# Kernel optimization log

Hardware: AMD Instinct MI355X
Metric: run time of the kernel (lower is better)

Reference implementation:

```python
import jax, jax.numpy as jnp
import numpy as np

RES = 64      # resolution (D=H=W)
WIDTH = 32    # FNO channel width
MODES = 8     # retained Fourier modes per dim
NL = 4        # FNO layers
NU = 0.000185 # viscosity
FCH = 128     # projection hidden width
B = 4


def setup_inputs() -> dict:
    key = jax.random.key(0)
    ks = jax.random.split(key, 8)
    u = jax.random.normal(ks[0], (B, 3, RES, RES, RES), jnp.float32)
    s = 1.0 / (WIDTH * WIDTH)
    fc0_w = jax.random.normal(ks[1], (3, WIDTH), jnp.float32) * (1.0 / 3.0) ** 0.5
    fc0_b = jnp.zeros((WIDTH,), jnp.float32)
    # (layer, corner, in, out, m1, m2, m3, re/im)
    spec_w = jax.random.normal(ks[2], (NL, 4, WIDTH, WIDTH, MODES, MODES, MODES, 2), jnp.float32) * s
    w_pw = jax.random.normal(ks[3], (NL, WIDTH, WIDTH), jnp.float32) * (1.0 / WIDTH) ** 0.5
    b_pw = jnp.zeros((NL, WIDTH), jnp.float32)
    fc1_w = jax.random.normal(ks[4], (WIDTH, FCH), jnp.float32) * (1.0 / WIDTH) ** 0.5
    fc1_b = jnp.zeros((FCH,), jnp.float32)
    fc2_w = jax.random.normal(ks[5], (FCH, 6), jnp.float32) * (1.0 / FCH) ** 0.5
    fc2_b = jnp.zeros((6,), jnp.float32)
    return dict(u=u, fc0_w=fc0_w, fc0_b=fc0_b, spec_w=spec_w, w_pw=w_pw,
                b_pw=b_pw, fc1_w=fc1_w, fc1_b=fc1_b, fc2_w=fc2_w, fc2_b=fc2_b)


def _pointwise(x, w, b):
    # 1x1x1 conv: (B,C,D,H,W) x (C,O) -> (B,O,D,H,W)
    return jnp.einsum('bcdhw,co->bodhw', x, w) + b[None, :, None, None, None]


def _spectral_conv(x, wf):
    m = MODES
    Bn, C, D, H, W = x.shape
    ft = jnp.fft.rfftn(x, axes=(-3, -2, -1))           # (B,C,D,H,W//2+1) complex64
    w = wf[..., 0] + 1j * wf[..., 1]                   # (4,C,O,m,m,m)
    mul = lambda blk, ww: jnp.einsum('bixyz,ioxyz->boxyz', blk, ww)
    out = jnp.zeros((Bn, w.shape[2], D, H, W // 2 + 1), jnp.complex64)
    out = out.at[:, :, :m, :m, :m].set(mul(ft[:, :, :m, :m, :m], w[0]))
    out = out.at[:, :, -m:, :m, :m].set(mul(ft[:, :, -m:, :m, :m], w[1]))
    out = out.at[:, :, :m, -m:, :m].set(mul(ft[:, :, :m, -m:, :m], w[2]))
    out = out.at[:, :, -m:, -m:, :m].set(mul(ft[:, :, -m:, -m:, :m], w[3]))
    return jnp.fft.irfftn(out, s=(D, H, W), axes=(-3, -2, -1))


def _fno(u, fc0_w, fc0_b, spec_w, w_pw, b_pw, fc1_w, fc1_b, fc2_w, fc2_b):
    x = _pointwise(u, fc0_w, fc0_b)
    for l in range(NL):
        x1 = _spectral_conv(x, spec_w[l])
        x2 = _pointwise(x, w_pw[l], b_pw[l])
        x = x1 + x2
        if l < NL - 1:
            x = jax.nn.gelu(x)
    x = jax.nn.gelu(_pointwise(x, fc1_w, fc1_b))
    return _pointwise(x, fc2_w, fc2_b)


def _ns_hard_core(u):
    # du/dt = -(u.grad)u + nu * lap(u), periodic central differences
    dx = 2.0 * np.pi / RES
    conv = jnp.zeros_like(u)
    diff = jnp.zeros_like(u)
    for j in range(3):
        ax = 2 + j
        up = jnp.roll(u, -1, axis=ax)
        um = jnp.roll(u, 1, axis=ax)
        du = (up - um) / (2.0 * dx)          # d u_i / d x_j for all i
        conv = conv - u[:, j:j + 1] * du
        diff = diff + (up - 2.0 * u + um) / (dx * dx)
    return conv + NU * diff


def reference(u, fc0_w, fc0_b, spec_w, w_pw, b_pw, fc1_w, fc1_b, fc2_w, fc2_b):
    du_hard = _ns_hard_core(u)
    tau = _fno(u, fc0_w, fc0_b, spec_w, w_pw, b_pw, fc1_w, fc1_b, fc2_w, fc2_b)
    du_dt = du_hard + tau[:, :3] * 0.001
    return du_dt, tau
```

## Files before the change

kernel.cpp:

```cpp
#include <hip/hip_runtime.h>
#include <hip/hip_bf16.h>

#define RES 64
#define WIDTH 32
#define MODES 8
#define R3 262144
#define TWO_PI_OVER_64 0.09817477042468103f

__device__ __forceinline__ float geluf(float x) {
    float g = 1.5957691216057308f * (x + 0.044715f * x * x * x);
    return x * __builtin_amdgcn_rcpf(1.0f + __expf(-g));
}

constexpr double tcos_(double x) {
    double r = 1.0, term = 1.0;
    for (int i = 1; i <= 12; i++) { term *= -x * x / ((2.0 * i - 1.0) * (2.0 * i)); r += term; }
    return r;
}
constexpr double tsin_(double x) {
    double r = x, term = x;
    for (int i = 1; i <= 12; i++) { term *= -x * x / ((2.0 * i) * (2.0 * i + 1.0)); r += term; }
    return r;
}
struct Tw64 { float c[64]; float s[64]; };
constexpr Tw64 mkTw() {
    Tw64 t{};
    const double th = 6.283185307179586476925286766559 / 64.0;
    for (int i = 0; i < 64; i++) {
        double a = th * (i <= 32 ? i : i - 64);
        t.c[i] = (float)tcos_(a);
        t.s[i] = (float)tsin_(a);
    }
    return t;
}
constexpr Tw64 TWT = mkTw();

__global__ void k_fc0(const float* __restrict__ u, const float* __restrict__ w,
                      const float* __restrict__ bias, float* __restrict__ X) {
    __shared__ float ws[96];
    __shared__ float bs[32];
    int t = threadIdx.x;
    if (t < 96) ws[t] = w[t];
    if (t < 32) bs[t] = bias[t];
    __syncthreads();
    size_t s = (size_t)blockIdx.x * 256 + t;
    int b = (int)(s >> 18);
    size_t p = s & (R3 - 1);
    const float* ub = u + (size_t)b * 3 * R3;
    float u0 = ub[p], u1 = ub[R3 + p], u2 = ub[2 * R3 + p];
    float* xb = X + (size_t)b * 32 * R3;
    #pragma unroll
    for (int o = 0; o < 32; o++) {
        xb[(size_t)o * R3 + p] = bs[o] + u0 * ws[o] + u1 * ws[32 + o] + u2 * ws[64 + o];
    }
}

__global__ void __launch_bounds__(256, 6)
k_fwd_zy(const float* __restrict__ X, float2* __restrict__ S2) {
    int t = threadIdx.x;
    int q = t >> 6, y = t & 63;
    int bcx0 = blockIdx.x * 4;
    __shared__ float2 zt[4][8][66];
    __shared__ float2 tw[64];
    if (t < 64) { float s, c; __sincosf(TWO_PI_OVER_64 * t, &s, &c); tw[t] = make_float2(c, s); }

    const float* row = X + (size_t)(bcx0 + q) * 4096 + (size_t)y * 64;
    float re[8], im[8];
    #pragma unroll
    for (int k = 0; k < 8; k++) { re[k] = 0.f; im[k] = 0.f; }
    #pragma unroll
    for (int zb = 0; zb < 8; zb++) {
        float xa[4], xb4[4];
        *(float4*)xa  = *(const float4*)(row + zb * 4);
        *(float4*)xb4 = *(const float4*)(row + zb * 4 + 32);
        #pragma unroll
        for (int j = 0; j < 4; j++) {
            int z = zb * 4 + j;
            float sv = xa[j] + xb4[j];
            float dv = xa[j] - xb4[j];
            #pragma unroll
            for (int k = 0; k < 8; k++) {
                float v = (k & 1) ? dv : sv;
                re[k] += v * TWT.c[(k * z) & 63];
                im[k] -= v * TWT.s[(k * z) & 63];
            }
        }
    }
    #pragma unroll
    for (int k = 0; k < 8; k++) zt[q][k][y] = make_float2(re[k], im[k]);
    __syncthreads();

    int l = t & 63;
    int jy = l >> 2, kp = l & 3;
    int f = jy < 8 ? jy : 48 + jy;
    int k0 = kp * 2;
    float re0 = 0.f, im0 = 0.f, re1 = 0.f, im1 = 0.f;
    #pragma unroll 8
    for (int yy = 0; yy < 64; yy++) {
        float2 w = tw[(f * yy) & 63];
        float2 v0 = zt[q][k0][yy];
        float2 v1 = zt[q][k0 + 1][yy];
        re0 += v0.x * w.x + v0.y * w.y;
        im0 += v0.y * w.x - v0.x * w.y;
        re1 += v1.x * w.x + v1.y * w.y;
        im1 += v1.y * w.x - v1.x * w.y;
    }
    float2* dst = S2 + (size_t)(bcx0 + q) * 128 + jy * 8 + k0;
    dst[0] = make_float2(re0, im0);
    dst[1] = make_float2(re1, im1);
}

__global__ void k_fwd_x(const float2* __restrict__ S2, float2* __restrict__ S3) {
    int bc = blockIdx.x >> 3, kz = blockIdx.x & 7;
    int t = threadIdx.x;
    __shared__ float2 in[64 * 16];
    __shared__ float2 tw[64];
    if (t < 64) { float s, c; __sincosf(TWO_PI_OVER_64 * t, &s, &c); tw[t] = make_float2(c, s); }
    #pragma unroll
    for (int i = 0; i < 4; i++) {
        int e = t + 256 * i;
        in[e] = S2[((size_t)bc * 1024 + e) * 8 + kz];
    }
    __syncthreads();
    int jx = t >> 4, jy = t & 15;
    int f = jx < 8 ? jx : 48 + jx;
    float re = 0.f, im = 0.f;
    for (int x = 0; x < 64; x++) {
        float2 v = in[x * 16 + jy];
        float2 w = tw[(f * x) & 63];
        re += v.x * w.x + v.y * w.y;
        im += v.y * w.x - v.x * w.y;
    }
    S3[(size_t)bc * 2048 + (size_t)t * 8 + kz] = make_float2(re, im);
}

__global__ void k_specmul(const float2* __restrict__ S3, const float* __restrict__ spec_w,
                          float2* __restrict__ S4, int layer) {
    int mp = blockIdx.x;
    int t = threadIdx.x;
    int jxy = mp >> 2;
    int kz0 = (mp & 3) * 2;
    int jy = jxy & 15, jx = jxy >> 4;
    int corner = (jx >= 8 ? 1 : 0) + (jy >= 8 ? 2 : 0);
    int m1 = jx & 7, m2 = jy & 7;
    int mode0 = jxy * 8 + kz0;
    __shared__ float4 W4[1024];
    __shared__ float2 inb[2][128];
    const float* wbase = spec_w + (size_t)layer * 4194304 + (size_t)corner * 1048576
                       + m1 * 128 + m2 * 16 + kz0 * 2;
    #pragma unroll
    for (int j = 0; j < 8; j++) {
        int e = t + 128 * j;
        int i = e >> 5, o = e & 31;
        W4[e] = *(const float4*)(wbase + (size_t)i * 32768 + (size_t)o * 1024);
    }
    inb[0][t] = S3[(size_t)t * 2048 + mode0];
    inb[1][t] = S3[(size_t)t * 2048 + mode0 + 1];
    __syncthreads();
    int b = t >> 5, o = t & 31;
    float re0 = 0.f, im0 = 0.f, re1 = 0.f, im1 = 0.f;
    #pragma unroll 8
    for (int i = 0; i < 32; i++) {
        float2 a0 = inb[0][b * 32 + i];
        float2 a1 = inb[1][b * 32 + i];
        float4 w = W4[i * 32 + o];
        re0 += a0.x * w.x - a0.y * w.y;
        im0 += a0.x * w.y + a0.y * w.x;
        re1 += a1.x * w.z - a1.y * w.w;
        im1 += a1.x * w.w + a1.y * w.z;
    }
    S4[(size_t)(b * 32 + o) * 2048 + mode0]     = make_float2(re0, im0);
    S4[(size_t)(b * 32 + o) * 2048 + mode0 + 1] = make_float2(re1, im1);
}

__global__ void k_inv_x(const float2* __restrict__ S4, float2* __restrict__ S5) {
    int bo = blockIdx.x >> 3, kz = blockIdx.x & 7;
    int t = threadIdx.x;
    __shared__ float2 in[256];
    __shared__ float2 tw[64];
    if (t < 64) { float s, c; __sincosf(TWO_PI_OVER_64 * t, &s, &c); tw[t] = make_float2(c, s); }
    in[t] = S4[(size_t)bo * 2048 + (size_t)t * 8 + kz];
    __syncthreads();
    int x = t & 63, g = t >> 6;
    #pragma unroll
    for (int m = 0; m < 4; m++) {
        int jy = g + 4 * m;
        float re = 0.f, im = 0.f;
        #pragma unroll
        for (int jx = 0; jx < 16; jx++) {
            int f = jx < 8 ? jx : 48 + jx;
            float2 v = in[jx * 16 + jy];
            float2 w = tw[(f * x) & 63];
            re += v.x * w.x - v.y * w.y;
            im += v.x * w.y + v.y * w.x;
        }
        S5[((size_t)bo * 64 + x) * 128 + jy * 8 + kz] = make_float2(re, im);
    }
}

__global__ void __launch_bounds__(256, 3)
k_inv_yz_pw(const float2* __restrict__ S5, const float* __restrict__ w_pw,
            const float* __restrict__ b_pw, float* __restrict__ X,
            int layer, int do_gelu) {
    int blk = blockIdx.x;
    int yg = blk & 3, x = (blk >> 2) & 63, b = blk >> 8;
    int t = threadIdx.x;
    __shared__ float2 s5s[32 * 132];
    __shared__ float2 st[256];
    __shared__ float xt[2048];
    __shared__ float2 tw[64];
    if (t < 64) { float s, c; __sincosf(TWO_PI_OVER_64 * t, &s, &c); tw[t] = make_float2(c, s); }
    #pragma unroll
    for (int i = 0; i < 8; i++) {
        int f4 = t + 256 * i;
        int o = f4 >> 6, j4 = f4 & 63;
        float4 v = ((const float4*)(S5 + ((size_t)(b * 32 + o) * 64 + x) * 128))[j4];
        *(float4*)(&s5s[o * 132 + j4 * 2]) = v;
    }
    __syncthreads();
    int z = t & 63, og = t >> 6;
    int og8 = og * 8;
    int og8u = __builtin_amdgcn_readfirstlane(og8);
    const float* wl = w_pw + layer * 1024 + og8u;
    const float* bl = b_pw + layer * 32 + og8u;
    float bt0 = bl[0], bt1 = bl[1], bt2 = bl[2], bt3 = bl[3];
    float bt4 = bl[4], bt5 = bl[5], bt6 = bl[6], bt7 = bl[7];
    float2 tz1 = tw[z];
    float2 tz2 = tw[(2 * z) & 63];
    float2 tz3 = tw[(3 * z) & 63];
    float2 tz4 = tw[(4 * z) & 63];
    float2 tz5 = tw[(5 * z) & 63];
    float2 tz6 = tw[(6 * z) & 63];
    float2 tz7 = tw[(7 * z) & 63];
    const float inv_n = 1.0f / 262144.0f;
    for (int yi = 0; yi < 16; yi++) {
        int y = yg * 16 + yi;
        {
            int o = t >> 3, k = t & 7;
            float re = 0.f, im = 0.f;
            #pragma unroll
            for (int jy = 0; jy < 16; jy++) {
                int f = jy < 8 ? jy : 48 + jy;
                float2 v = s5s[o * 132 + jy * 8 + k];
                float2 w = tw[(f * y) & 63];
                re += v.x * w.x - v.y * w.y;
                im += v.x * w.y + v.y * w.x;
            }
            st[t] = make_float2(re, im);
        }
        size_t base = (size_t)b * 8388608 + (size_t)(x * 64 + y) * 64;
        #pragma unroll
        for (int i = 0; i < 8; i++) {
            int e = t + 256 * i;
            int c = e >> 6, zz = e & 63;
            xt[e] = X[base + (size_t)c * R3 + zz];
        }
        __syncthreads();
#define INVZ_S(o) (st[(o) * 8 + 0].x \
        + 2.f * (st[(o) * 8 + 1].x * tz1.x - st[(o) * 8 + 1].y * tz1.y) \
        + 2.f * (st[(o) * 8 + 2].x * tz2.x - st[(o) * 8 + 2].y * tz2.y) \
        + 2.f * (st[(o) * 8 + 3].x * tz3.x - st[(o) * 8 + 3].y * tz3.y) \
        + 2.f * (st[(o) * 8 + 4].x * tz4.x - st[(o) * 8 + 4].y * tz4.y) \
        + 2.f * (st[(o) * 8 + 5].x * tz5.x - st[(o) * 8 + 5].y * tz5.y) \
        + 2.f * (st[(o) * 8 + 6].x * tz6.x - st[(o) * 8 + 6].y * tz6.y) \
        + 2.f * (st[(o) * 8 + 7].x * tz7.x - st[(o) * 8 + 7].y * tz7.y))
        float acc0 = bt0 + INVZ_S(og8 + 0) * inv_n;
        float acc1 = bt1 + INVZ_S(og8 + 1) * inv_n;
        float acc2 = bt2 + INVZ_S(og8 + 2) * inv_n;
        float acc3 = bt3 + INVZ_S(og8 + 3) * inv_n;
        float acc4 = bt4 + INVZ_S(og8 + 4) * inv_n;
        float acc5 = bt5 + INVZ_S(og8 + 5) * inv_n;
        float acc6 = bt6 + INVZ_S(og8 + 6) * inv_n;
        float acc7 = bt7 + INVZ_S(og8 + 7) * inv_n;
#undef INVZ_S
        #pragma unroll 4
        for (int c = 0; c < 32; c++) {
            float xc = xt[c * 64 + z];
            const float* wr = wl + c * 32;
            float w0 = wr[0], w1 = wr[1], w2 = wr[2], w3 = wr[3];
            float w4 = wr[4], w5 = wr[5], w6 = wr[6], w7 = wr[7];
            acc0 += xc * w0; acc1 += xc * w1; acc2 += xc * w2; acc3 += xc * w3;
            acc4 += xc * w4; acc5 += xc * w5; acc6 += xc * w6; acc7 += xc * w7;
        }
        __syncthreads();
        float r;
        r = do_gelu ? geluf(acc0) : acc0; X[base + (size_t)(og8 + 0) * R3 + z] = r;
        r = do_gelu ? geluf(acc1) : acc1; X[base + (size_t)(og8 + 1) * R3 + z] = r;
        r = do_gelu ? geluf(acc2) : acc2; X[base + (size_t)(og8 + 2) * R3 + z] = r;
        r = do_gelu ? geluf(acc3) : acc3; X[base + (size_t)(og8 + 3) * R3 + z] = r;
        r = do_gelu ? geluf(acc4) : acc4; X[base + (size_t)(og8 + 4) * R3 + z] = r;
        r = do_gelu ? geluf(acc5) : acc5; X[base + (size_t)(og8 + 5) * R3 + z] = r;
        r = do_gelu ? geluf(acc6) : acc6; X[base + (size_t)(og8 + 6) * R3 + z] = r;
        r = do_gelu ? geluf(acc7) : acc7; X[base + (size_t)(og8 + 7) * R3 + z] = r;
    }
}

#define X32(M) M(0) M(1) M(2) M(3) M(4) M(5) M(6) M(7) M(8) M(9) M(10) M(11) M(12) M(13) \
               M(14) M(15) M(16) M(17) M(18) M(19) M(20) M(21) M(22) M(23) M(24) M(25) \
               M(26) M(27) M(28) M(29) M(30) M(31)
__global__ void __launch_bounds__(256, 2)
k_head(const float* __restrict__ X, const float* __restrict__ w1,
       const float* __restrict__ b1, const float* __restrict__ w2,
       const float* __restrict__ b2, float* __restrict__ tau_out) {
    int t = threadIdx.x;
    size_t s0 = ((size_t)blockIdx.x * 256 + t) * 2;
    int b = (int)(s0 >> 18);
    size_t p = s0 & (R3 - 1);
    const float* xb = X + (size_t)b * 8388608 + p;
#define LOADX(c) float2 v##c = *(const float2*)(xb + (size_t)(c) * R3);
    X32(LOADX)
#undef LOADX
    float acc00 = b2[0], acc01 = b2[1], acc02 = b2[2], acc03 = b2[3], acc04 = b2[4], acc05 = b2[5];
    float acc10 = acc00, acc11 = acc01, acc12 = acc02, acc13 = acc03, acc14 = acc04, acc15 = acc05;
    for (int h = 0; h < 128; h += 4) {
        float a00 = b1[h], a01 = b1[h + 1], a02 = b1[h + 2], a03 = b1[h + 3];
        float a10 = a00, a11 = a01, a12 = a02, a13 = a03;
#define FMA_C(c) { float4 w = *(const float4*)(w1 + (c) * 128 + h); \
        a00 += v##c.x * w.x; a01 += v##c.x * w.y; a02 += v##c.x * w.z; a03 += v##c.x * w.w; \
        a10 += v##c.y * w.x; a11 += v##c.y * w.y; a12 += v##c.y * w.z; a13 += v##c.y * w.w; }
        X32(FMA_C)
#undef FMA_C
        a00 = geluf(a00); a01 = geluf(a01); a02 = geluf(a02); a03 = geluf(a03);
        a10 = geluf(a10); a11 = geluf(a11); a12 = geluf(a12); a13 = geluf(a13);
        const float* w2r = w2 + h * 6;
        acc00 += a00 * w2r[0] + a01 * w2r[6] + a02 * w2r[12] + a03 * w2r[18];
        acc01 += a00 * w2r[1] + a01 * w2r[7] + a02 * w2r[13] + a03 * w2r[19];
        acc02 += a00 * w2r[2] + a01 * w2r[8] + a02 * w2r[14] + a03 * w2r[20];
        acc03 += a00 * w2r[3] + a01 * w2r[9] + a02 * w2r[15] + a03 * w2r[21];
        acc04 += a00 * w2r[4] + a01 * w2r[10] + a02 * w2r[16] + a03 * w2r[22];
        acc05 += a00 * w2r[5] + a01 * w2r[11] + a02 * w2r[17] + a03 * w2r[23];
        acc10 += a10 * w2r[0] + a11 * w2r[6] + a12 * w2r[12] + a13 * w2r[18];
        acc11 += a10 * w2r[1] + a11 * w2r[7] + a12 * w2r[13] + a13 * w2r[19];
        acc12 += a10 * w2r[2] + a11 * w2r[8] + a12 * w2r[14] + a13 * w2r[20];
        acc13 += a10 * w2r[3] + a11 * w2r[9] + a12 * w2r[15] + a13 * w2r[21];
        acc14 += a10 * w2r[4] + a11 * w2r[10] + a12 * w2r[16] + a13 * w2r[22];
        acc15 += a10 * w2r[5] + a11 * w2r[11] + a12 * w2r[17] + a13 * w2r[23];
    }
    float* ob = tau_out + (size_t)b * 6 * R3 + p;
    *(float2*)(ob + (size_t)0 * R3) = make_float2(acc00, acc10);
    *(float2*)(ob + (size_t)1 * R3) = make_float2(acc01, acc11);
    *(float2*)(ob + (size_t)2 * R3) = make_float2(acc02, acc12);
    *(float2*)(ob + (size_t)3 * R3) = make_float2(acc03, acc13);
    *(float2*)(ob + (size_t)4 * R3) = make_float2(acc04, acc14);
    *(float2*)(ob + (size_t)5 * R3) = make_float2(acc05, acc15);
}

__global__ void k_hard(const float* __restrict__ u, const float* __restrict__ tau,
                       float* __restrict__ out0) {
    size_t s = (size_t)blockIdx.x * 256 + threadIdx.x;
    int bi = (int)(s >> 18);
    int b = bi / 3, i = bi % 3;
    size_t p = s & (R3 - 1);
    int x = (int)(p >> 12), y = ((int)p >> 6) & 63, z = (int)p & 63;
    const float dx = TWO_PI_OVER_64;
    const float inv2dx = 1.0f / (2.0f * dx);
    const float invdx2 = 1.0f / (dx * dx);
    const float* ub = u + (size_t)b * 3 * R3;
    const float* ui = ub + (size_t)i * R3;
    int xp = (x + 1) & 63, xm = (x + 63) & 63;
    int yp = (y + 1) & 63, ym = (y + 63) & 63;
    int zp = (z + 1) & 63, zm = (z + 63) & 63;
    float c0 = ui[p];
    float upx = ui[((size_t)xp << 12) | (y << 6) | z], umx = ui[((size_t)xm << 12) | (y << 6) | z];
    float upy = ui[((size_t)x << 12) | (yp << 6) | z], umy = ui[((size_t)x << 12) | (ym << 6) | z];
    float upz = ui[((size_t)x << 12) | (y << 6) | zp], umz = ui[((size_t)x << 12) | (y << 6) | zm];
    float u0c = ub[p], u1c = ub[R3 + p], u2c = ub[2 * R3 + p];
    float conv = -(u0c * (upx - umx) + u1c * (upy - umy) + u2c * (upz - umz)) * inv2dx;
    float diff = (upx + umx + upy + umy + upz + umz - 6.0f * c0) * invdx2;
    float tauv = tau[(size_t)b * 6 * R3 + (size_t)i * R3 + p];
    out0[s] = conv + 0.000185f * diff + 0.001f * tauv;
}

extern "C" void kernel_launch(void* const* d_in, const int* in_sizes, int n_in,
                              void* d_out, int out_size, void* d_ws, size_t ws_size,
                              hipStream_t stream) {
    const float* u      = (const float*)d_in[0];
    const float* fc0_w  = (const float*)d_in[1];
    const float* fc0_b  = (const float*)d_in[2];
    const float* spec_w = (const float*)d_in[3];
    const float* w_pw   = (const float*)d_in[4];
    const float* b_pw   = (const float*)d_in[5];
    const float* fc1_w  = (const float*)d_in[6];
    const float* fc1_b  = (const float*)d_in[7];
    const float* fc2_w  = (const float*)d_in[8];
    const float* fc2_b  = (const float*)d_in[9];
    float* out = (float*)d_out;

    float* X = (float*)d_ws;

    float2* S2 = (float2*)(out);
    float2* S3 = (float2*)(out + 2097152);
    float2* S4 = (float2*)(out + 2621440);
    float2* S5 = (float2*)(out + 3145728);

    k_fc0<<<4096, 256, 0, stream>>>(u, fc0_w, fc0_b, X);

    for (int l = 0; l < 4; l++) {
        k_fwd_zy<<<2048, 256, 0, stream>>>(X, S2);
        k_fwd_x<<<1024, 256, 0, stream>>>(S2, S3);
        k_specmul<<<1024, 128, 0, stream>>>(S3, spec_w, S4, l);
        k_inv_x<<<1024, 256, 0, stream>>>(S4, S5);
        k_inv_yz_pw<<<1024, 256, 0, stream>>>(S5, w_pw, b_pw, X, l, (l < 3) ? 1 : 0);
    }

    float* tau_out = out + (size_t)4 * 3 * R3;
    k_head<<<2048, 256, 0, stream>>>(X, fc1_w, fc1_b, fc2_w, fc2_b, tau_out);
    k_hard<<<12288, 256, 0, stream>>>(u, tau_out, out);
}
```

Before: 1.170 ms.

## Use bf16x3 split MFMA for projection head matmul with DPP reductions

Rewrites the projection head kernel so the 32->128 fc1 matmul runs on MFMA 16x16x32 bf16 instructions. Each fp32 value is split into a high and a low bf16 part, and three products are summed to stay close to fp32 accuracy. The 128->6 fc2 step is spread across lanes and reduced with DPP row shuffles, and the grid is doubled so each thread handles fewer points. The aim is to cut the large scalar FMA load of the head, at the cost of extra split/convert work, cross-lane reductions, and some precision risk.

```diff
diff --git a/kernel.cpp b/kernel.cpp
--- a/kernel.cpp
+++ b/kernel.cpp
@@ -295,54 +295,110 @@
     }
 }
 
-#define X32(M) M(0) M(1) M(2) M(3) M(4) M(5) M(6) M(7) M(8) M(9) M(10) M(11) M(12) M(13) \
-               M(14) M(15) M(16) M(17) M(18) M(19) M(20) M(21) M(22) M(23) M(24) M(25) \
-               M(26) M(27) M(28) M(29) M(30) M(31)
+typedef short bf16x8_t __attribute__((ext_vector_type(8)));
+typedef float f32x4_t __attribute__((ext_vector_type(4)));
+
+__device__ __forceinline__ float dpp_add16(float v) {
+    int i;
+    i = __builtin_amdgcn_update_dpp(0, __builtin_bit_cast(int, v), 0xB1, 0xF, 0xF, true);
+    v += __builtin_bit_cast(float, i);
+    i = __builtin_amdgcn_update_dpp(0, __builtin_bit_cast(int, v), 0x4E, 0xF, 0xF, true);
+    v += __builtin_bit_cast(float, i);
+    i = __builtin_amdgcn_update_dpp(0, __builtin_bit_cast(int, v), 0x141, 0xF, 0xF, true);
+    v += __builtin_bit_cast(float, i);
+    i = __builtin_amdgcn_update_dpp(0, __builtin_bit_cast(int, v), 0x140, 0xF, 0xF, true);
+    v += __builtin_bit_cast(float, i);
+    return v;
+}
+
 __global__ void __launch_bounds__(256, 2)
 k_head(const float* __restrict__ X, const float* __restrict__ w1,
        const float* __restrict__ b1, const float* __restrict__ w2,
        const float* __restrict__ b2, float* __restrict__ tau_out) {
     int t = threadIdx.x;
-    size_t s0 = ((size_t)blockIdx.x * 256 + t) * 2;
-    int b = (int)(s0 >> 18);
-    size_t p = s0 & (R3 - 1);
-    const float* xb = X + (size_t)b * 8388608 + p;
-#define LOADX(c) float2 v##c = *(const float2*)(xb + (size_t)(c) * R3);
-    X32(LOADX)
-#undef LOADX
-    float acc00 = b2[0], acc01 = b2[1], acc02 = b2[2], acc03 = b2[3], acc04 = b2[4], acc05 = b2[5];
-    float acc10 = acc00, acc11 = acc01, acc12 = acc02, acc13 = acc03, acc14 = acc04, acc15 = acc05;
-    for (int h = 0; h < 128; h += 4) {
-        float a00 = b1[h], a01 = b1[h + 1], a02 = b1[h + 2], a03 = b1[h + 3];
-        float a10 = a00, a11 = a01, a12 = a02, a13 = a03;
-#define FMA_C(c) { float4 w = *(const float4*)(w1 + (c) * 128 + h); \
-        a00 += v##c.x * w.x; a01 += v##c.x * w.y; a02 += v##c.x * w.z; a03 += v##c.x * w.w; \
-        a10 += v##c.y * w.x; a11 += v##c.y * w.y; a12 += v##c.y * w.z; a13 += v##c.y * w.w; }
-        X32(FMA_C)
-#undef FMA_C
-        a00 = geluf(a00); a01 = geluf(a01); a02 = geluf(a02); a03 = geluf(a03);
-        a10 = geluf(a10); a11 = geluf(a11); a12 = geluf(a12); a13 = geluf(a13);
-        const float* w2r = w2 + h * 6;
-        acc00 += a00 * w2r[0] + a01 * w2r[6] + a02 * w2r[12] + a03 * w2r[18];
-        acc01 += a00 * w2r[1] + a01 * w2r[7] + a02 * w2r[13] + a03 * w2r[19];
-        acc02 += a00 * w2r[2] + a01 * w2r[8] + a02 * w2r[14] + a03 * w2r[20];
-        acc03 += a00 * w2r[3] + a01 * w2r[9] + a02 * w2r[15] + a03 * w2r[21];
-        acc04 += a00 * w2r[4] + a01 * w2r[10] + a02 * w2r[16] + a03 * w2r[22];
-        acc05 += a00 * w2r[5] + a01 * w2r[11] + a02 * w2r[17] + a03 * w2r[23];
-        acc10 += a10 * w2r[0] + a11 * w2r[6] + a12 * w2r[12] + a13 * w2r[18];
-        acc11 += a10 * w2r[1] + a11 * w2r[7] + a12 * w2r[13] + a13 * w2r[19];
-        acc12 += a10 * w2r[2] + a11 * w2r[8] + a12 * w2r[14] + a13 * w2r[20];
-        acc13 += a10 * w2r[3] + a11 * w2r[9] + a12 * w2r[15] + a13 * w2r[21];
-        acc14 += a10 * w2r[4] + a11 * w2r[10] + a12 * w2r[16] + a13 * w2r[22];
-        acc15 += a10 * w2r[5] + a11 * w2r[11] + a12 * w2r[17] + a13 * w2r[23];
-    }
-    float* ob = tau_out + (size_t)b * 6 * R3 + p;
-    *(float2*)(ob + (size_t)0 * R3) = make_float2(acc00, acc10);
-    *(float2*)(ob + (size_t)1 * R3) = make_float2(acc01, acc11);
-    *(float2*)(ob + (size_t)2 * R3) = make_float2(acc02, acc12);
-    *(float2*)(ob + (size_t)3 * R3) = make_float2(acc03, acc13);
-    *(float2*)(ob + (size_t)4 * R3) = make_float2(acc04, acc14);
-    *(float2*)(ob + (size_t)5 * R3) = make_float2(acc05, acc15);
+    int lane = t & 63;
+    int wv = t >> 6;
+    int m = lane & 15;
+    int g = lane >> 4;
+    size_t sblock = (size_t)blockIdx.x * 256;
+    int b = (int)(sblock >> 18);
+    size_t pblock = sblock & (R3 - 1);
+    const float* xb = X + (size_t)b * 8388608 + pblock;
+
+    bf16x8_t Bhi[8], Blo[8];
+    #pragma unroll
+    for (int tt = 0; tt < 8; tt++) {
+        #pragma unroll
+        for (int j = 0; j < 8; j++) {
+            float w = w1[(g * 8 + j) * 128 + tt * 16 + m];
+            unsigned bits = __builtin_bit_cast(unsigned, w);
+            float hf = __builtin_bit_cast(float, bits & 0xFFFF0000u);
+            float lof = w - hf;
+            unsigned lb = __builtin_bit_cast(unsigned, lof);
+            Bhi[tt][j] = (short)(bits >> 16);
+            Blo[tt][j] = (short)(lb >> 16);
+        }
+    }
+    float w2r[8][6];
+    #pragma unroll
+    for (int tt = 0; tt < 8; tt++)
+        #pragma unroll
+        for (int o = 0; o < 6; o++) w2r[tt][o] = w2[(tt * 16 + m) * 6 + o];
+    float b1r[8];
+    #pragma unroll
+    for (int tt = 0; tt < 8; tt++) b1r[tt] = b1[tt * 16 + m];
+    float b2m = b2[m < 6 ? m : 0];
+
+    for (int it = 0; it < 4; it++) {
+        int s16 = wv * 64 + it * 16;
+        bf16x8_t Ahi, Alo;
+        #pragma unroll
+        for (int j = 0; j < 8; j++) {
+            float xv = xb[(size_t)(g * 8 + j) * R3 + s16 + m];
+            unsigned bits = __builtin_bit_cast(unsigned, xv);
+            float hf = __builtin_bit_cast(float, bits & 0xFFFF0000u);
+            float lof = xv - hf;
+            unsigned lb = __builtin_bit_cast(unsigned, lof);
+            Ahi[j] = (short)(bits >> 16);
+            Alo[j] = (short)(lb >> 16);
+        }
+        float p0[6] = {0.f, 0.f, 0.f, 0.f, 0.f, 0.f};
+        float p1[6] = {0.f, 0.f, 0.f, 0.f, 0.f, 0.f};
+        float p2[6] = {0.f, 0.f, 0.f, 0.f, 0.f, 0.f};
+        float p3[6] = {0.f, 0.f, 0.f, 0.f, 0.f, 0.f};
+        #pragma unroll
+        for (int tt = 0; tt < 8; tt++) {
+            f32x4_t d = {0.f, 0.f, 0.f, 0.f};
+            d = __builtin_amdgcn_mfma_f32_16x16x32_bf16(Ahi, Bhi[tt], d, 0, 0, 0);
+            d = __builtin_amdgcn_mfma_f32_16x16x32_bf16(Ahi, Blo[tt], d, 0, 0, 0);
+            d = __builtin_amdgcn_mfma_f32_16x16x32_bf16(Alo, Bhi[tt], d, 0, 0, 0);
+            float a0 = geluf(d[0] + b1r[tt]);
+            float a1 = geluf(d[1] + b1r[tt]);
+            float a2 = geluf(d[2] + b1r[tt]);
+            float a3 = geluf(d[3] + b1r[tt]);
+            #pragma unroll
+            for (int o = 0; o < 6; o++) {
+                float w = w2r[tt][o];
+                p0[o] += a0 * w; p1[o] += a1 * w; p2[o] += a2 * w; p3[o] += a3 * w;
+            }
+        }
+        float q0 = 0.f, q1 = 0.f, q2 = 0.f, q3 = 0.f;
+        #pragma unroll
+        for (int o = 0; o < 6; o++) {
+            float r0 = dpp_add16(p0[o]);
+            float r1 = dpp_add16(p1[o]);
+            float r2 = dpp_add16(p2[o]);
+            float r3 = dpp_add16(p3[o]);
+            q0 = (m == o) ? r0 : q0;
+            q1 = (m == o) ? r1 : q1;
+            q2 = (m == o) ? r2 : q2;
+            q3 = (m == o) ? r3 : q3;
+        }
+        if (m < 6) {
+            float4 vv = make_float4(q0 + b2m, q1 + b2m, q2 + b2m, q3 + b2m);
+            *(float4*)(tau_out + (size_t)b * 6 * R3 + (size_t)m * R3 + pblock + s16 + g * 4) = vv;
+        }
+    }
 }
 
 __global__ void k_hard(const float* __restrict__ u, const float* __restrict__ tau,
@@ -404,6 +460,6 @@
     }
 
     float* tau_out = out + (size_t)4 * 3 * R3;
-    k_head<<<2048, 256, 0, stream>>>(X, fc1_w, fc1_b, fc2_w, fc2_b, tau_out);
+    k_head<<<4096, 256, 0, stream>>>(X, fc1_w, fc1_b, fc2_w, fc2_b, tau_out);
     k_hard<<<12288, 256, 0, stream>>>(u, tau_out, out);
 }
```

After: 1.123 ms. 1.04x faster.
